# Kernel optimization log

Measured on AMD Instinct MI355X. Metric: run time of the kernel, lower is better.

The kernel has to match this reference:

```python
import jax, jax.numpy as jnp
import numpy as np

D_MODEL = 2048
NUM_HEADS = 16
HEAD_DIM = D_MODEL // NUM_HEADS  # 128
ROPE_BASE = 10000.0
B, L = 2, 2048


def _rope_tables(seq_len, head_dim, base):
    # inv_freq over even dims; cos/sin tables of shape (seq_len, head_dim)
    inv_freq = 1.0 / (base ** (jnp.arange(0, head_dim, 2, dtype=jnp.float32) / head_dim))
    t = jnp.arange(seq_len, dtype=jnp.float32)
    freqs = jnp.einsum('l,d->ld', t, inv_freq)          # (L, head_dim/2)
    emb = jnp.concatenate([freqs, freqs], axis=-1)       # (L, head_dim)
    return jnp.cos(emb), jnp.sin(emb)


def _apply_rope(x, cos, sin):
    # x: (B, H, L, d); rotate-half convention
    d = x.shape[-1]
    x1, x2 = x[..., : d // 2], x[..., d // 2:]
    rotated = jnp.concatenate([-x2, x1], axis=-1)
    return x * cos + rotated * sin


def setup_inputs() -> dict:
    key = jax.random.key(0)
    k0, k1, k2 = jax.random.split(key, 3)
    query = jax.random.normal(k0, (B, L, D_MODEL), dtype=jnp.float32)
    W_qkv = jax.random.normal(k1, (3 * D_MODEL, D_MODEL), dtype=jnp.float32) * 0.02
    b_qkv = jnp.zeros((3 * D_MODEL,), dtype=jnp.float32)
    W_out = jax.random.normal(k2, (D_MODEL, D_MODEL), dtype=jnp.float32) * 0.02
    b_out = jnp.zeros((D_MODEL,), dtype=jnp.float32)
    return {"query": query, "W_qkv": W_qkv, "b_qkv": b_qkv, "W_out": W_out, "b_out": b_out}


def reference(query, W_qkv, b_qkv, W_out, b_out):
    Bq, Lq, _ = query.shape
    # fused QKV projection (single matmul)
    qkv = jnp.einsum('bld,ed->ble', query, W_qkv) + b_qkv  # (B, L, 3D)
    q, k, v = jnp.split(qkv, 3, axis=-1)

    def shape_heads(x):
        return x.reshape(Bq, Lq, NUM_HEADS, HEAD_DIM).transpose(0, 2, 1, 3)  # (B,H,L,d)

    q, k, v = shape_heads(q), shape_heads(k), shape_heads(v)

    cos, sin = _rope_tables(Lq, HEAD_DIM, ROPE_BASE)
    q = _apply_rope(q, cos, sin)
    k = _apply_rope(k, cos, sin)

    scale = 1.0 / jnp.sqrt(jnp.asarray(HEAD_DIM, dtype=q.dtype))
    scores = jnp.einsum('bhqd,bhkd->bhqk', q, k) * scale  # (B,H,L,L)
    causal = jnp.tril(jnp.ones((Lq, Lq), dtype=bool))
    scores = jnp.where(causal, scores, jnp.finfo(scores.dtype).min)
    probs = jax.nn.softmax(scores, axis=-1)
    attn = jnp.einsum('bhqk,bhkd->bhqd', probs, v)        # (B,H,L,d)

    out = attn.transpose(0, 2, 1, 3).reshape(Bq, Lq, D_MODEL)
    return jnp.einsum('bld,ed->ble', out, W_out) + b_out
```

## Files before the change

### kernel.cpp

```cpp
#include <hip/hip_runtime.h>

typedef unsigned short u16;
typedef unsigned int u32;
typedef __bf16 bf16x8 __attribute__((ext_vector_type(8)));
typedef float f32x4 __attribute__((ext_vector_type(4)));

__device__ __forceinline__ u16 f2b(float f) {
  u32 u = __float_as_uint(f);
  u32 r = (u + 0x7fffu + ((u >> 16) & 1u)) >> 16;
  return (u16)r;
}
__device__ __forceinline__ float b2f(u16 v) {
  return __uint_as_float(((u32)v) << 16);
}

__global__ __launch_bounds__(256) void convert_all(
    const float4* __restrict__ q, const float4* __restrict__ w1,
    const float4* __restrict__ w2, ushort4* __restrict__ out) {
  int i = blockIdx.x * 256 + threadIdx.x;
  float4 f;
  if (i < 2097152) f = q[i];
  else if (i < 5242880) f = w1[i - 2097152];
  else f = w2[i - 5242880];
  ushort4 o;
  o.x = f2b(f.x); o.y = f2b(f.y); o.z = f2b(f.z); o.w = f2b(f.w);
  out[i] = o;
}

__global__ __launch_bounds__(256) void rope_tab(float2* __restrict__ tab) {
  int idx = blockIdx.x * 256 + threadIdx.x;
  int l = idx >> 6, dp = idx & 63;
  float inv = exp2f(-(float)dp * 0.20762050593046869f);
  float ang = (float)l * inv;
  float s, c;
  sincosf(ang, &s, &c);
  tab[idx] = make_float2(c, s);
}

__global__ __launch_bounds__(256) void gemm_qkv(
    const u16* __restrict__ A, const u16* __restrict__ B,
    const float* __restrict__ bias, const float2* __restrict__ tab,
    u16* __restrict__ qh, u16* __restrict__ kh, u16* __restrict__ vhT) {
  __shared__ __align__(16) u16 sh[16512];
  u16* As = sh;
  u16* Bs = sh + 8192;
  const int K = 2048;
  const int tid = threadIdx.x;
  const int lane = tid & 63;
  const int wave = tid >> 6;
  const int m0 = blockIdx.y * 128;
  const int n0 = blockIdx.x * 128;
  const int wm = (wave & 1) * 64;
  const int wn = (wave >> 1) * 64;
  f32x4 acc[4][4] = {};

  const int srow = wave * 32 + (lane >> 3);
  const int scb = ((lane & 7) ^ (lane >> 3)) * 16;
  const int fr = lane & 15;
  const int g = lane >> 4;

  for (int kt = 0; kt < 32; ++kt) {
    const int k0 = kt << 6;
    __syncthreads();
    {
      const char* gA = (const char*)A + ((size_t)(m0 + srow) * K + k0) * 2 + scb;
      const char* gB = (const char*)B + ((size_t)(n0 + srow) * K + k0) * 2 + scb;
#pragma unroll
      for (int i = 0; i < 4; ++i) {
        __builtin_amdgcn_global_load_lds(
            (__attribute__((address_space(1))) void*)(gA + (size_t)i * 8 * K * 2),
            (__attribute__((address_space(3))) void*)(As + (wave * 32 + i * 8) * 64),
            16, 0, 0);
        __builtin_amdgcn_global_load_lds(
            (__attribute__((address_space(1))) void*)(gB + (size_t)i * 8 * K * 2),
            (__attribute__((address_space(3))) void*)(Bs + (wave * 32 + i * 8) * 64),
            16, 0, 0);
      }
    }
    __syncthreads();
#pragma unroll
    for (int ks = 0; ks < 2; ++ks) {
      const int so = ((ks * 4 + g) ^ (fr & 7)) * 8;
      bf16x8 aF[4], bF[4];
#pragma unroll
      for (int mi = 0; mi < 4; ++mi)
        __builtin_memcpy(&aF[mi], &As[(wm + mi * 16 + fr) * 64 + so], 16);
#pragma unroll
      for (int ni = 0; ni < 4; ++ni)
        __builtin_memcpy(&bF[ni], &Bs[(wn + ni * 16 + fr) * 64 + so], 16);
#pragma unroll
      for (int mi = 0; mi < 4; ++mi)
#pragma unroll
        for (int ni = 0; ni < 4; ++ni)
          acc[mi][ni] = __builtin_amdgcn_mfma_f32_16x16x32_bf16(aF[mi], bF[ni], acc[mi][ni], 0, 0, 0);
    }
  }

  __syncthreads();
  const int rq = (lane >> 4) * 4;
  const int cq = lane & 15;
#pragma unroll
  for (int mi = 0; mi < 4; ++mi) {
#pragma unroll
    for (int ni = 0; ni < 4; ++ni) {
      int c = wn + ni * 16 + cq;
      float bs = bias[n0 + c];
#pragma unroll
      for (int i = 0; i < 4; ++i) {
        int r = wm + mi * 16 + rq + i;
        sh[r * 129 + c] = f2b(acc[mi][ni][i] + bs);
      }
    }
  }
  __syncthreads();

  const int t = n0 >> 7;
  const int h = t & 15;
  const int bq = m0 >> 11;
  const int l0 = m0 & 2047;
  const int bh = bq * 16 + h;

  if (t < 32) {
    const float qs = (t < 16) ? 0.08838834764831845f : 1.0f;
    u16* dst = (t < 16) ? qh : kh;
#pragma unroll 4
    for (int it = 0; it < 32; ++it) {
      int idx = it * 256 + tid;
      int l = idx >> 6, dp = idx & 63;
      float2 cs = tab[(size_t)(l0 + l) * 64 + dp];
      float x1 = b2f(sh[l * 129 + dp]);
      float x2 = b2f(sh[l * 129 + dp + 64]);
      size_t o = ((size_t)bh * 2048 + l0 + l) * 128;
      dst[o + dp]      = f2b((x1 * cs.x - x2 * cs.y) * qs);
      dst[o + dp + 64] = f2b((x2 * cs.x + x1 * cs.y) * qs);
    }
  } else {
#pragma unroll 4
    for (int it = 0; it < 32; ++it) {
      int idx = it * 256 + tid;
      int d = idx >> 6, l2 = (idx & 63) * 2;
      ushort2 t2;
      t2.x = sh[l2 * 129 + d];
      t2.y = sh[(l2 + 1) * 129 + d];
      *(ushort2*)(vhT + ((size_t)bh * 128 + d) * 2048 + l0 + l2) = t2;
    }
  }
}

__global__ __launch_bounds__(256) void gemm_bt(
    const u16* __restrict__ A, const u16* __restrict__ B,
    const float* __restrict__ bias, float* __restrict__ C,
    int M, int N, int K) {
  __shared__ __align__(16) u16 As[128 * 64];
  __shared__ __align__(16) u16 Bs[128 * 64];
  const int tid = threadIdx.x;
  const int lane = tid & 63;
  const int wave = tid >> 6;
  const int m0 = blockIdx.y * 128;
  const int n0 = blockIdx.x * 128;
  const int wm = (wave & 1) * 64;
  const int wn = (wave >> 1) * 64;
  f32x4 acc[4][4] = {};

  const int srow = wave * 32 + (lane >> 3);
  const int scb = ((lane & 7) ^ (lane >> 3)) * 16;
  const int fr = lane & 15;
  const int g = lane >> 4;

  const int kiters = K >> 6;
  for (int kt = 0; kt < kiters; ++kt) {
    const int k0 = kt << 6;
    __syncthreads();
    {
      const char* gA = (const char*)A + ((size_t)(m0 + srow) * K + k0) * 2 + scb;
      const char* gB = (const char*)B + ((size_t)(n0 + srow) * K + k0) * 2 + scb;
#pragma unroll
      for (int i = 0; i < 4; ++i) {
        __builtin_amdgcn_global_load_lds(
            (__attribute__((address_space(1))) void*)(gA + (size_t)i * 8 * K * 2),
            (__attribute__((address_space(3))) void*)(As + (wave * 32 + i * 8) * 64),
            16, 0, 0);
        __builtin_amdgcn_global_load_lds(
            (__attribute__((address_space(1))) void*)(gB + (size_t)i * 8 * K * 2),
            (__attribute__((address_space(3))) void*)(Bs + (wave * 32 + i * 8) * 64),
            16, 0, 0);
      }
    }
    __syncthreads();
#pragma unroll
    for (int ks = 0; ks < 2; ++ks) {
      const int so = ((ks * 4 + g) ^ (fr & 7)) * 8;
      bf16x8 aF[4], bF[4];
#pragma unroll
      for (int mi = 0; mi < 4; ++mi)
        __builtin_memcpy(&aF[mi], &As[(wm + mi * 16 + fr) * 64 + so], 16);
#pragma unroll
      for (int ni = 0; ni < 4; ++ni)
        __builtin_memcpy(&bF[ni], &Bs[(wn + ni * 16 + fr) * 64 + so], 16);
#pragma unroll
      for (int mi = 0; mi < 4; ++mi)
#pragma unroll
        for (int ni = 0; ni < 4; ++ni)
          acc[mi][ni] = __builtin_amdgcn_mfma_f32_16x16x32_bf16(aF[mi], bF[ni], acc[mi][ni], 0, 0, 0);
    }
  }
  const int rq = (lane >> 4) * 4;
  const int cq = lane & 15;
#pragma unroll
  for (int mi = 0; mi < 4; ++mi) {
#pragma unroll
    for (int ni = 0; ni < 4; ++ni) {
      int col = n0 + wn + ni * 16 + cq;
      float bs = bias[col];
#pragma unroll
      for (int i = 0; i < 4; ++i) {
        int row = m0 + wm + mi * 16 + rq + i;
        C[(size_t)row * N + col] = acc[mi][ni][i] + bs;
      }
    }
  }
}

__global__ __launch_bounds__(256, 2) void attn_flash(
    const u16* __restrict__ qh, const u16* __restrict__ kh,
    const u16* __restrict__ vhT, u16* __restrict__ oh) {
  __shared__ __align__(16) u16 Ks[64 * 128];
  __shared__ __align__(16) u16 Vt[128 * 64];
  __shared__ __align__(16) u16 Ps[128 * 72];
  const int tid = threadIdx.x;
  const int lane = tid & 63;
  const int w = tid >> 6;
  const int cq = lane & 15;
  const int g = lane >> 4;
  const int p = blockIdx.x;
  const int bh = blockIdx.y;
  const int b = bh >> 4, h = bh & 15;
  const int ktiles = 32 - p;
  int q0s[2];
  q0s[0] = p * 64;
  q0s[1] = (31 - p) * 64;

  bf16x8 qf[2][4];
#pragma unroll
  for (int s = 0; s < 2; ++s) {
    const u16* qp = qh + ((size_t)bh * 2048 + q0s[s] + w * 16 + cq) * 128 + g * 8;
#pragma unroll
    for (int ks = 0; ks < 4; ++ks)
      __builtin_memcpy(&qf[s][ks], qp + ks * 32, 16);
  }

  f32x4 o[2][8] = {};
  float mrow[2] = {-1e30f, -1e30f};
  float lrow[2] = {0.0f, 0.0f};

  const int krl = lane >> 4;
  const int kcl = lane & 15;
  const int vrl = lane >> 3;
  const int vcl = lane & 7;

  for (int kt = 0; kt < ktiles; ++kt) {
    __syncthreads();
    {
      const size_t kvb = (size_t)bh * 2048 + (size_t)kt * 64;
#pragma unroll
      for (int i = 0; i < 4; ++i) {
        int row = w * 16 + i * 4 + krl;
        int cgl = kcl ^ (row & 7);
        const char* src = (const char*)(kh + (kvb + row) * 128 + cgl * 8);
        __builtin_amdgcn_global_load_lds(
            (__attribute__((address_space(1))) void*)src,
            (__attribute__((address_space(3))) void*)(Ks + (w * 16 + i * 4) * 128),
            16, 0, 0);
      }
#pragma unroll
      for (int i = 0; i < 4; ++i) {
        int row = w * 32 + i * 8 + vrl;
        int cgl = vcl ^ (row & 7);
        const char* src =
            (const char*)(vhT + ((size_t)bh * 128 + row) * 2048 + kt * 64 + cgl * 8);
        __builtin_amdgcn_global_load_lds(
            (__attribute__((address_space(1))) void*)src,
            (__attribute__((address_space(3))) void*)(Vt + (w * 32 + i * 8) * 64),
            16, 0, 0);
      }
    }
    __syncthreads();

    const bool nA = (kt <= p);
    f32x4 S[4][2] = {};
#pragma unroll
    for (int ks = 0; ks < 4; ++ks) {
#pragma unroll
      for (int mt = 0; mt < 4; ++mt) {
        bf16x8 kf;
        int slot = (ks * 4 + g) ^ (cq & 7);
        __builtin_memcpy(&kf, &Ks[(mt * 16 + cq) * 128 + slot * 8], 16);
        if (nA)
          S[mt][0] = __builtin_amdgcn_mfma_f32_16x16x32_bf16(kf, qf[0][ks], S[mt][0], 0, 0, 0);
        S[mt][1] = __builtin_amdgcn_mfma_f32_16x16x32_bf16(kf, qf[1][ks], S[mt][1], 0, 0, 0);
      }
    }

#pragma unroll
    for (int s = 0; s < 2; ++s) {
      if (s == 0 && !nA) continue;
      const int dtile = s ? (ktiles - 1) : p;
      if (kt == dtile) {
        const int qg = q0s[s] + w * 16 + cq;
#pragma unroll
        for (int mt = 0; mt < 4; ++mt)
#pragma unroll
          for (int i = 0; i < 4; ++i)
            if (kt * 64 + mt * 16 + g * 4 + i > qg) S[mt][s][i] = -1e30f;
      }
      float mx = S[0][s][0];
#pragma unroll
      for (int mt = 0; mt < 4; ++mt)
#pragma unroll
        for (int i = 0; i < 4; ++i) mx = fmaxf(mx, S[mt][s][i]);
      mx = fmaxf(mx, __shfl_xor(mx, 16));
      mx = fmaxf(mx, __shfl_xor(mx, 32));
      float mnew = fmaxf(mrow[s], mx);
      float al = __expf(mrow[s] - mnew);
      mrow[s] = mnew;
      float rs = 0.0f;
#pragma unroll
      for (int mt = 0; mt < 4; ++mt) {
        float e0 = __expf(S[mt][s][0] - mnew);
        float e1 = __expf(S[mt][s][1] - mnew);
        float e2 = __expf(S[mt][s][2] - mnew);
        float e3 = __expf(S[mt][s][3] - mnew);
        rs += (e0 + e1) + (e2 + e3);
        ushort4 pk;
        pk.x = f2b(e0); pk.y = f2b(e1); pk.z = f2b(e2); pk.w = f2b(e3);
        *(ushort4*)&Ps[(s * 64 + w * 16 + cq) * 72 + mt * 16 + g * 4] = pk;
      }
      rs += __shfl_xor(rs, 16);
      rs += __shfl_xor(rs, 32);
      lrow[s] = lrow[s] * al + rs;
#pragma unroll
      for (int dmt = 0; dmt < 8; ++dmt) {
        o[s][dmt][0] *= al; o[s][dmt][1] *= al;
        o[s][dmt][2] *= al; o[s][dmt][3] *= al;
      }
    }

#pragma unroll
    for (int ks = 0; ks < 2; ++ks) {
      bf16x8 pf0, pf1;
      if (nA) __builtin_memcpy(&pf0, &Ps[(w * 16 + cq) * 72 + ks * 32 + g * 8], 16);
      __builtin_memcpy(&pf1, &Ps[(64 + w * 16 + cq) * 72 + ks * 32 + g * 8], 16);
#pragma unroll
      for (int dmt = 0; dmt < 8; ++dmt) {
        bf16x8 vf;
        int slot = (ks * 4 + g) ^ (cq & 7);
        __builtin_memcpy(&vf, &Vt[(dmt * 16 + cq) * 64 + slot * 8], 16);
        if (nA)
          o[0][dmt] = __builtin_amdgcn_mfma_f32_16x16x32_bf16(vf, pf0, o[0][dmt], 0, 0, 0);
        o[1][dmt] = __builtin_amdgcn_mfma_f32_16x16x32_bf16(vf, pf1, o[1][dmt], 0, 0, 0);
      }
    }
  }

#pragma unroll
  for (int s = 0; s < 2; ++s) {
    float inv = 1.0f / lrow[s];
    int qg = q0s[s] + w * 16 + cq;
    size_t base = ((size_t)(b * 2048 + qg)) * 2048 + h * 128;
#pragma unroll
    for (int dmt = 0; dmt < 8; ++dmt) {
      ushort4 t;
      t.x = f2b(o[s][dmt][0] * inv);
      t.y = f2b(o[s][dmt][1] * inv);
      t.z = f2b(o[s][dmt][2] * inv);
      t.w = f2b(o[s][dmt][3] * inv);
      *(ushort4*)(oh + base + dmt * 16 + g * 4) = t;
    }
  }
}

extern "C" void kernel_launch(void* const* d_in, const int* in_sizes, int n_in,
                              void* d_out, int out_size, void* d_ws, size_t ws_size,
                              hipStream_t stream) {
  (void)in_sizes; (void)n_in; (void)out_size; (void)ws_size;
  const float* query = (const float*)d_in[0];
  const float* W_qkv = (const float*)d_in[1];
  const float* b_qkv = (const float*)d_in[2];
  const float* W_out = (const float*)d_in[3];
  const float* b_out = (const float*)d_in[4];
  float* out = (float*)d_out;
  char* ws = (char*)d_ws;

  u16*    Abf  = (u16*)(ws + 0);
  u16*    W1bf = (u16*)(ws + (size_t)16777216);
  u16*    W2bf = (u16*)(ws + (size_t)41943040);
  u16*    qhp  = (u16*)(ws + (size_t)50331648);
  u16*    khp  = (u16*)(ws + (size_t)67108864);
  u16*    vhT  = (u16*)(ws + (size_t)83886080);
  u16*    ohp  = (u16*)(ws + (size_t)100663296);
  float2* tab  = (float2*)(ws + (size_t)117440512);

  convert_all<<<24576, 256, 0, stream>>>((const float4*)query, (const float4*)W_qkv,
                                         (const float4*)W_out, (ushort4*)ws);
  rope_tab<<<512, 256, 0, stream>>>(tab);
  gemm_qkv<<<dim3(48, 32), 256, 0, stream>>>(Abf, W1bf, b_qkv, tab, qhp, khp, vhT);
  attn_flash<<<dim3(16, 32), 256, 0, stream>>>(qhp, khp, vhT, ohp);
  gemm_bt<<<dim3(16, 32), 256, 0, stream>>>(ohp, W2bf, b_out, out, 4096, 2048, 2048);
}
```

Baseline: 381.4 us.

## Rewrite QKV GEMM as 256x256 double-buffered, 8-wave pipelined tile with swizzled block order

```diff
diff --git a/kernel.cpp b/kernel.cpp
--- a/kernel.cpp
+++ b/kernel.cpp
@@ -37,112 +37,164 @@
   tab[idx] = make_float2(c, s);
 }
 
-__global__ __launch_bounds__(256) void gemm_qkv(
+__global__ __launch_bounds__(512, 2) void gemm_qkv(
     const u16* __restrict__ A, const u16* __restrict__ B,
     const float* __restrict__ bias, const float2* __restrict__ tab,
     u16* __restrict__ qh, u16* __restrict__ kh, u16* __restrict__ vhT) {
-  __shared__ __align__(16) u16 sh[16512];
-  u16* As = sh;
-  u16* Bs = sh + 8192;
+  __shared__ __align__(16) u16 sh[65536];
   const int K = 2048;
   const int tid = threadIdx.x;
   const int lane = tid & 63;
-  const int wave = tid >> 6;
-  const int m0 = blockIdx.y * 128;
-  const int n0 = blockIdx.x * 128;
-  const int wm = (wave & 1) * 64;
-  const int wn = (wave >> 1) * 64;
-  f32x4 acc[4][4] = {};
-
-  const int srow = wave * 32 + (lane >> 3);
-  const int scb = ((lane & 7) ^ (lane >> 3)) * 16;
+  const int w = tid >> 6;
   const int fr = lane & 15;
   const int g = lane >> 4;
 
-  for (int kt = 0; kt < 32; ++kt) {
-    const int k0 = kt << 6;
-    __syncthreads();
-    {
-      const char* gA = (const char*)A + ((size_t)(m0 + srow) * K + k0) * 2 + scb;
-      const char* gB = (const char*)B + ((size_t)(n0 + srow) * K + k0) * 2 + scb;
-#pragma unroll
-      for (int i = 0; i < 4; ++i) {
-        __builtin_amdgcn_global_load_lds(
-            (__attribute__((address_space(1))) void*)(gA + (size_t)i * 8 * K * 2),
-            (__attribute__((address_space(3))) void*)(As + (wave * 32 + i * 8) * 64),
-            16, 0, 0);
-        __builtin_amdgcn_global_load_lds(
-            (__attribute__((address_space(1))) void*)(gB + (size_t)i * 8 * K * 2),
-            (__attribute__((address_space(3))) void*)(Bs + (wave * 32 + i * 8) * 64),
-            16, 0, 0);
-      }
-    }
-    __syncthreads();
-#pragma unroll
-    for (int ks = 0; ks < 2; ++ks) {
-      const int so = ((ks * 4 + g) ^ (fr & 7)) * 8;
-      bf16x8 aF[4], bF[4];
+  int wid = blockIdx.y * 24 + blockIdx.x;
+  wid = (wid & 7) * 48 + (wid >> 3);
+  const int m0 = (wid / 24) * 256;
+  const int n0 = (wid % 24) * 256;
+
+  const int sr = tid >> 3;
+  const int scb = ((tid & 7) ^ (sr & 7)) * 16;
+
+  auto STAGE = [&](const u16* src, int grow0, int k0, int slot) {
+    const char* gp = (const char*)src + ((size_t)(grow0 + sr) * K + k0) * 2 + scb;
+#pragma unroll
+    for (int i = 0; i < 2; ++i)
+      __builtin_amdgcn_global_load_lds(
+          (__attribute__((address_space(1))) void*)(gp + (size_t)i * 64 * K * 2),
+          (__attribute__((address_space(3))) void*)(sh + slot + i * 4096 + w * 512),
+          16, 0, 0);
+  };
+  auto LDA = [&](bf16x8 (&dst)[4][2], int slot) {
+#pragma unroll
+    for (int mi = 0; mi < 4; ++mi)
+#pragma unroll
+      for (int ks = 0; ks < 2; ++ks)
+        __builtin_memcpy(&dst[mi][ks],
+            &sh[slot + ((w & 1) * 64 + mi * 16 + fr) * 64 + (((ks * 4 + g) ^ (fr & 7)) * 8)],
+            16);
+  };
+  auto LDB = [&](bf16x8 (&dst)[2][2], int slot) {
+#pragma unroll
+    for (int ni = 0; ni < 2; ++ni)
+#pragma unroll
+      for (int ks = 0; ks < 2; ++ks)
+        __builtin_memcpy(&dst[ni][ks],
+            &sh[slot + ((w >> 1) * 32 + ni * 16 + fr) * 64 + (((ks * 4 + g) ^ (fr & 7)) * 8)],
+            16);
+  };
+
+  f32x4 acc[8][4] = {};
+  auto MMA = [&](bf16x8 (&af)[4][2], bf16x8 (&bf)[2][2], int mo, int no) {
+    __builtin_amdgcn_s_setprio(1);
+#pragma unroll
+    for (int ks = 0; ks < 2; ++ks)
 #pragma unroll
       for (int mi = 0; mi < 4; ++mi)
-        __builtin_memcpy(&aF[mi], &As[(wm + mi * 16 + fr) * 64 + so], 16);
-#pragma unroll
-      for (int ni = 0; ni < 4; ++ni)
-        __builtin_memcpy(&bF[ni], &Bs[(wn + ni * 16 + fr) * 64 + so], 16);
-#pragma unroll
-      for (int mi = 0; mi < 4; ++mi)
-#pragma unroll
-        for (int ni = 0; ni < 4; ++ni)
-          acc[mi][ni] = __builtin_amdgcn_mfma_f32_16x16x32_bf16(aF[mi], bF[ni], acc[mi][ni], 0, 0, 0);
-    }
-  }
-
-  __syncthreads();
-  const int rq = (lane >> 4) * 4;
-  const int cq = lane & 15;
-#pragma unroll
-  for (int mi = 0; mi < 4; ++mi) {
-#pragma unroll
-    for (int ni = 0; ni < 4; ++ni) {
-      int c = wn + ni * 16 + cq;
-      float bs = bias[n0 + c];
-#pragma unroll
-      for (int i = 0; i < 4; ++i) {
-        int r = wm + mi * 16 + rq + i;
-        sh[r * 129 + c] = f2b(acc[mi][ni][i] + bs);
-      }
-    }
-  }
-  __syncthreads();
-
-  const int t = n0 >> 7;
-  const int h = t & 15;
-  const int bq = m0 >> 11;
-  const int l0 = m0 & 2047;
-  const int bh = bq * 16 + h;
-
-  if (t < 32) {
-    const float qs = (t < 16) ? 0.08838834764831845f : 1.0f;
-    u16* dst = (t < 16) ? qh : kh;
+#pragma unroll
+        for (int ni = 0; ni < 2; ++ni)
+          acc[mo + mi][no + ni] = __builtin_amdgcn_mfma_f32_16x16x32_bf16(
+              af[mi][ks], bf[ni][ks], acc[mo + mi][no + ni], 0, 0, 0);
+    __builtin_amdgcn_s_setprio(0);
+  };
+
+  STAGE(A, m0, 0, 0);
+  STAGE(B, n0, 0, 16384);
+  STAGE(A, m0 + 128, 0, 8192);
+  STAGE(B, n0 + 128, 0, 24576);
+  STAGE(A, m0, 64, 32768);
+  STAGE(B, n0, 64, 32768 + 16384);
+  STAGE(A, m0 + 128, 64, 32768 + 8192);
+  asm volatile("s_waitcnt vmcnt(6)" ::: "memory");
+  __builtin_amdgcn_s_barrier();
+
+  for (int t = 0; t < 32; ++t) {
+    const int buf = (t & 1) << 15;
+    const int nbuf = buf ^ 32768;
+    const int k2 = (t + 2) << 6;
+    bf16x8 aF[4][2], bF0[2][2], bF1[2][2];
+
+    LDA(aF, buf);
+    LDB(bF0, buf + 16384);
+    if (t + 1 < 32) STAGE(B, n0 + 128, (t + 1) << 6, nbuf + 24576);
+    __builtin_amdgcn_s_barrier();
+    MMA(aF, bF0, 0, 0);
+    __builtin_amdgcn_s_barrier();
+
+    LDB(bF1, buf + 24576);
+    if (t + 2 < 32) STAGE(A, m0, k2, buf);
+    __builtin_amdgcn_s_barrier();
+    MMA(aF, bF1, 0, 2);
+    __builtin_amdgcn_s_barrier();
+
+    LDA(aF, buf + 8192);
+    if (t + 2 < 32) STAGE(B, n0, k2, buf + 16384);
+    __builtin_amdgcn_s_barrier();
+    MMA(aF, bF1, 4, 2);
+    __builtin_amdgcn_s_barrier();
+
+    if (t + 2 < 32) {
+      STAGE(A, m0 + 128, k2, buf + 8192);
+      asm volatile("s_waitcnt vmcnt(6)" ::: "memory");
+    } else {
+      asm volatile("s_waitcnt vmcnt(0)" ::: "memory");
+    }
+    __builtin_amdgcn_s_barrier();
+    MMA(aF, bF0, 4, 0);
+    __builtin_amdgcn_s_barrier();
+  }
+
+  const int rq = g * 4;
+  const int cq = fr;
+#pragma unroll
+  for (int nh = 0; nh < 2; ++nh) {
+    __syncthreads();
+#pragma unroll
+    for (int m = 0; m < 8; ++m) {
+#pragma unroll
+      for (int nl = 0; nl < 2; ++nl) {
+        const int n = nh * 2 + nl;
+        const int c = (w >> 1) * 32 + nl * 16 + cq;
+        const float bs = bias[n0 + nh * 128 + c];
+        const int rb = (m >> 2) * 128 + (w & 1) * 64 + (m & 3) * 16 + rq;
+#pragma unroll
+        for (int i = 0; i < 4; ++i)
+          sh[(rb + i) * 129 + c] = f2b(acc[m][n][i] + bs);
+      }
+    }
+    __syncthreads();
+
+    const int th = (n0 >> 7) + nh;
+    const int h = th & 15;
+    const int bq = m0 >> 11;
+    const int l0 = m0 & 2047;
+    const int bh = bq * 16 + h;
+
+    if (th < 32) {
+      const float qs2 = (th < 16) ? 0.08838834764831845f : 1.0f;
+      u16* dst = (th < 16) ? qh : kh;
 #pragma unroll 4
-    for (int it = 0; it < 32; ++it) {
-      int idx = it * 256 + tid;
-      int l = idx >> 6, dp = idx & 63;
-      float2 cs = tab[(size_t)(l0 + l) * 64 + dp];
-      float x1 = b2f(sh[l * 129 + dp]);
-      float x2 = b2f(sh[l * 129 + dp + 64]);
-      size_t o = ((size_t)bh * 2048 + l0 + l) * 128;
-      dst[o + dp]      = f2b((x1 * cs.x - x2 * cs.y) * qs);
-      dst[o + dp + 64] = f2b((x2 * cs.x + x1 * cs.y) * qs);
-    }
-  } else {
+      for (int it = 0; it < 32; ++it) {
+        int idx = it * 512 + tid;
+        int l = idx >> 6, dp = idx & 63;
+        float2 cs = tab[(size_t)(l0 + l) * 64 + dp];
+        float x1 = b2f(sh[l * 129 + dp]);
+        float x2 = b2f(sh[l * 129 + dp + 64]);
+        size_t o = ((size_t)bh * 2048 + l0 + l) * 128;
+        dst[o + dp]      = f2b((x1 * cs.x - x2 * cs.y) * qs2);
+        dst[o + dp + 64] = f2b((x2 * cs.x + x1 * cs.y) * qs2);
+      }
+    } else {
 #pragma unroll 4
-    for (int it = 0; it < 32; ++it) {
-      int idx = it * 256 + tid;
-      int d = idx >> 6, l2 = (idx & 63) * 2;
-      ushort2 t2;
-      t2.x = sh[l2 * 129 + d];
-      t2.y = sh[(l2 + 1) * 129 + d];
-      *(ushort2*)(vhT + ((size_t)bh * 128 + d) * 2048 + l0 + l2) = t2;
+      for (int it = 0; it < 32; ++it) {
+        int idx = it * 512 + tid;
+        int d = idx >> 7, l2 = (idx & 127) * 2;
+        ushort2 t2;
+        t2.x = sh[l2 * 129 + d];
+        t2.y = sh[(l2 + 1) * 129 + d];
+        *(ushort2*)(vhT + ((size_t)bh * 128 + d) * 2048 + l0 + l2) = t2;
+      }
     }
   }
 }
@@ -288,6 +340,7 @@
 
     const bool nA = (kt <= p);
     f32x4 S[4][2] = {};
+    __builtin_amdgcn_s_setprio(1);
 #pragma unroll
     for (int ks = 0; ks < 4; ++ks) {
 #pragma unroll
@@ -300,6 +353,7 @@
         S[mt][1] = __builtin_amdgcn_mfma_f32_16x16x32_bf16(kf, qf[1][ks], S[mt][1], 0, 0, 0);
       }
     }
+    __builtin_amdgcn_s_setprio(0);
 
 #pragma unroll
     for (int s = 0; s < 2; ++s) {
@@ -345,6 +399,7 @@
       }
     }
 
+    __builtin_amdgcn_s_setprio(1);
 #pragma unroll
     for (int ks = 0; ks < 2; ++ks) {
       bf16x8 pf0, pf1;
@@ -360,6 +415,7 @@
         o[1][dmt] = __builtin_amdgcn_mfma_f32_16x16x32_bf16(vf, pf1, o[1][dmt], 0, 0, 0);
       }
     }
+    __builtin_amdgcn_s_setprio(0);
   }
 
 #pragma unroll
@@ -403,7 +459,7 @@
   convert_all<<<24576, 256, 0, stream>>>((const float4*)query, (const float4*)W_qkv,
                                          (const float4*)W_out, (ushort4*)ws);
   rope_tab<<<512, 256, 0, stream>>>(tab);
-  gemm_qkv<<<dim3(48, 32), 256, 0, stream>>>(Abf, W1bf, b_qkv, tab, qhp, khp, vhT);
+  gemm_qkv<<<dim3(24, 16), 512, 0, stream>>>(Abf, W1bf, b_qkv, tab, qhp, khp, vhT);
   attn_flash<<<dim3(16, 32), 256, 0, stream>>>(qhp, khp, vhT, ohp);
   gemm_bt<<<dim3(16, 32), 256, 0, stream>>>(ohp, W2bf, b_out, out, 4096, 2048, 2048);
 }
```

Result: slower. 421.5 us (+10.5%).
